# Optimization experiments

Hardware: AMD Instinct MI355X
Metric: run time of the kernel (lower is better)

The kernel has to match this reference:

```python
import jax, jax.numpy as jnp
import numpy as np

B, N, D = 256, 2048, 128
ANCHOR = 0


def setup_inputs() -> dict:
    key = jax.random.key(0)
    k0, k1, k2, k3 = jax.random.split(key, 4)
    return {
        "embs": jax.random.normal(k0, (B * N, D), jnp.float32),
        "W1": jax.random.normal(k1, (D, 2 * D), jnp.float32) / np.sqrt(2 * D),
        "b1": jnp.zeros((D,), jnp.float32),
        "W2": jax.random.normal(k2, (D, D), jnp.float32) / np.sqrt(D),
        "b2": jnp.zeros((D,), jnp.float32),
        "batch_idx": jax.random.randint(k3, (B * N,), 0, B, dtype=jnp.int32),
        "batch_size": B,
        "num_nodes": N,
        "num_anchors": ANCHOR,
    }


def reference(embs, W1, b1, W2, b2, batch_idx, batch_size, num_nodes, num_anchors):
    # static boolean mask over nodes (num_anchors is a Python int)
    non_target = np.arange(num_nodes) != num_anchors
    e = embs.reshape(batch_size, num_nodes, -1)            # (B, N, D)
    non_targets = e[:, non_target]                          # (B, N-1, D)
    target = e[:, ~non_target]                              # (B, 1, D)
    x = jnp.concatenate(
        (jnp.broadcast_to(target, non_targets.shape), non_targets), axis=-1
    )                                                       # (B, N-1, 2D)
    h = jax.nn.relu(jnp.einsum("bnk,dk->bnd", x, W1) + b1)  # (B, N-1, D)
    y = jnp.einsum("bnk,dk->bnd", h, W2) + b2               # (B, N-1, D)
    y = y.reshape(batch_size * (num_nodes - 1), -1)
    bidx = batch_idx.reshape(batch_size, num_nodes)[:, non_target].reshape(-1)
    return jax.ops.segment_sum(y, bidx, num_segments=batch_size)  # (B, D)
```

## Files before the change

kernel.cpp:

```cpp
#include <hip/hip_runtime.h>

#define B_SZ    256
#define N_NODES 2048
#define D_DIM   128
#define NROW_TOT (B_SZ * N_NODES)

typedef __attribute__((ext_vector_type(8))) short short8;
typedef __attribute__((ext_vector_type(4))) float f32x4;

#define WS_W1BF   0
#define WS_COUNT  65536
#define WS_OFF    66560
#define WS_CURSOR 67584
#define WS_ACC    83968
#define WS_P      215040
#define WS_NEEDED (WS_P + NROW_TOT * 4)

__device__ __forceinline__ unsigned pk2(float x, float y) {
    unsigned a = __float_as_uint(x), b = __float_as_uint(y);
    a += 0x7fffu + ((a >> 16) & 1u);
    b += 0x7fffu + ((b >> 16) & 1u);
    return (a >> 16) | (b & 0xffff0000u);
}

__global__ void k_prep_w1(const float* __restrict__ W1, unsigned* __restrict__ w1bf) {
    int i = blockIdx.x * 256 + threadIdx.x;
    float2 f = ((const float2*)W1)[i];
    w1bf[i] = pk2(f.x, f.y);
}

__global__ void k_hist(const int* __restrict__ bidx, int* __restrict__ count) {
    __shared__ int lh[256];
    int t = threadIdx.x;
    lh[t] = 0;
    __syncthreads();
    int base = blockIdx.x * 1024 + t * 4;
    int4 v = ((const int4*)bidx)[blockIdx.x * 256 + t];
    if (((base + 0) & 2047) != 0) atomicAdd(&lh[v.x], 1);
    if (((base + 1) & 2047) != 0) atomicAdd(&lh[v.y], 1);
    if (((base + 2) & 2047) != 0) atomicAdd(&lh[v.z], 1);
    if (((base + 3) & 2047) != 0) atomicAdd(&lh[v.w], 1);
    __syncthreads();
    if (lh[t]) atomicAdd(&count[t], lh[t]);
}

__global__ void k_scan(const int* __restrict__ count, int* __restrict__ off,
                       int* __restrict__ cursor) {
    __shared__ int sv[256];
    int t = threadIdx.x;
    sv[t] = count[t];
    __syncthreads();
    for (int o = 1; o < 256; o <<= 1) {
        int v = (t >= o) ? sv[t - o] : 0;
        __syncthreads();
        sv[t] += v;
        __syncthreads();
    }
    int ex = sv[t] - count[t];
    off[t] = ex;
    cursor[t * 16] = ex;
}

__global__ void k_scatter(const int* __restrict__ bidx, int* __restrict__ cursor,
                          int* __restrict__ P) {
    __shared__ int lh[256];
    __shared__ int sbase[256];
    int t = threadIdx.x;
    lh[t] = 0;
    __syncthreads();
    int base = blockIdx.x * 1024 + t * 4;
    int4 v = ((const int4*)bidx)[blockIdx.x * 256 + t];
    int p0 = -1, p1 = -1, p2 = -1, p3 = -1;
    if (((base + 0) & 2047) != 0) p0 = atomicAdd(&lh[v.x], 1);
    if (((base + 1) & 2047) != 0) p1 = atomicAdd(&lh[v.y], 1);
    if (((base + 2) & 2047) != 0) p2 = atomicAdd(&lh[v.z], 1);
    if (((base + 3) & 2047) != 0) p3 = atomicAdd(&lh[v.w], 1);
    __syncthreads();
    if (lh[t]) sbase[t] = atomicAdd(&cursor[t * 16], lh[t]);
    __syncthreads();
    if (p0 >= 0) P[sbase[v.x] + p0] = base + 0;
    if (p1 >= 0) P[sbase[v.y] + p1] = base + 1;
    if (p2 >= 0) P[sbase[v.z] + p2] = base + 2;
    if (p3 >= 0) P[sbase[v.w] + p3] = base + 3;
}

#define CHUNK   64
#define ESTRIDE 528

__global__ __launch_bounds__(1024) void k_main(
    const float* __restrict__ embs, const float* __restrict__ b1,
    const short* __restrict__ w1bf, const int* __restrict__ P,
    const int* __restrict__ off, const int* __restrict__ count,
    float* __restrict__ ACC)
{
    __shared__ char  estage[CHUNK * ESTRIDE];
    __shared__ float segacc[D_DIM];

    int tid = threadIdx.x;
    int s   = blockIdx.x;
    int cnt = count[s];
    int base = off[s];

    if (tid < D_DIM) segacc[tid] = 0.f;

    int lane = tid & 63;
    int wid  = tid >> 6;
    int rt   = wid & 3;
    int cg   = wid >> 2;
    int q    = lane >> 4;
    int i15  = lane & 15;

    short8 bfrag[8][2];
#pragma unroll
    for (int kt = 0; kt < 8; kt++)
#pragma unroll
        for (int ct = 0; ct < 2; ct++) {
            int n = cg * 32 + ct * 16 + i15;
            bfrag[kt][ct] = *(const short8*)(w1bf + n * 256 + kt * 32 + q * 8);
        }
    float b1c0 = b1[cg * 32 + i15];
    float b1c1 = b1[cg * 32 + 16 + i15];
    float asum0 = 0.f, asum1 = 0.f;

    int srow = tid >> 4;
    int part = tid & 15;
    __syncthreads();

    int nchunk = (cnt + CHUNK - 1) >> 6;
    for (int c = 0; c < nchunk; c++) {
        int rl = c * 64 + srow;
        int gr = base + (rl < cnt ? rl : cnt - 1);
        int ridx = P[gr];
        int b = ridx >> 11;
        const float4* src;
        if (part < 8) src = (const float4*)(embs + (b << 11) * D_DIM) + part * 4;
        else          src = (const float4*)(embs + ridx * D_DIM) + (part - 8) * 4;
        float4 f0 = src[0], f1 = src[1], f2 = src[2], f3 = src[3];
        unsigned u0 = pk2(f0.x, f0.y), u1 = pk2(f0.z, f0.w);
        unsigned u2 = pk2(f1.x, f1.y), u3 = pk2(f1.z, f1.w);
        unsigned u4 = pk2(f2.x, f2.y), u5 = pk2(f2.z, f2.w);
        unsigned u6 = pk2(f3.x, f3.y), u7 = pk2(f3.z, f3.w);
        uint4* dst = (uint4*)(estage + srow * ESTRIDE + part * 32);
        dst[0] = make_uint4(u0, u1, u2, u3);
        dst[1] = make_uint4(u4, u5, u6, u7);
        __syncthreads();

        f32x4 m0 = {0.f, 0.f, 0.f, 0.f}, m1 = {0.f, 0.f, 0.f, 0.f};
        const char* arow = estage + (rt * 16 + i15) * ESTRIDE + q * 16;
#pragma unroll
        for (int kt = 0; kt < 8; kt++) {
            short8 a = *(const short8*)(arow + kt * 64);
            m0 = __builtin_amdgcn_mfma_f32_16x16x32_bf16(a, bfrag[kt][0], m0, 0, 0, 0);
            m1 = __builtin_amdgcn_mfma_f32_16x16x32_bf16(a, bfrag[kt][1], m1, 0, 0, 0);
        }
        int rbase = c * 64 + rt * 16 + q * 4;
#pragma unroll
        for (int j = 0; j < 4; j++) {
            if (rbase + j < cnt) {
                asum0 += fmaxf(m0[j] + b1c0, 0.f);
                asum1 += fmaxf(m1[j] + b1c1, 0.f);
            }
        }
        __syncthreads();
    }

    asum0 += __shfl_xor(asum0, 16, 64);
    asum0 += __shfl_xor(asum0, 32, 64);
    asum1 += __shfl_xor(asum1, 16, 64);
    asum1 += __shfl_xor(asum1, 32, 64);
    if (lane < 16) {
        atomicAdd(&segacc[cg * 32 + lane],      asum0);
        atomicAdd(&segacc[cg * 32 + 16 + lane], asum1);
    }
    __syncthreads();
    if (tid < D_DIM) ACC[s * D_DIM + tid] = segacc[tid];
}

__global__ void k_out(const float* __restrict__ ACC, const float* __restrict__ W2,
                      const float* __restrict__ b2, const int* __restrict__ count,
                      float* __restrict__ out) {
    __shared__ float a[D_DIM];
    int s = blockIdx.x, d = threadIdx.x;
    a[d] = ACC[s * D_DIM + d];
    __syncthreads();
    float sum = (float)count[s] * b2[d];
    const float4* w = (const float4*)(W2 + d * D_DIM);
#pragma unroll
    for (int k = 0; k < 32; k++) {
        float4 wv = w[k];
        sum += a[4 * k + 0] * wv.x + a[4 * k + 1] * wv.y
             + a[4 * k + 2] * wv.z + a[4 * k + 3] * wv.w;
    }
    out[s * D_DIM + d] = sum;
}

extern "C" void kernel_launch(void* const* d_in, const int* in_sizes, int n_in,
                              void* d_out, int out_size, void* d_ws, size_t ws_size,
                              hipStream_t stream) {
    const float* embs = (const float*)d_in[0];
    const float* W1   = (const float*)d_in[1];
    const float* b1   = (const float*)d_in[2];
    const float* W2   = (const float*)d_in[3];
    const float* b2   = (const float*)d_in[4];
    const int*   bidx = (const int*)d_in[5];

    char* ws = (char*)d_ws;
    unsigned* w1bf_u = (unsigned*)(ws + WS_W1BF);
    short*    w1bf   = (short*)(ws + WS_W1BF);
    int*   count  = (int*)(ws + WS_COUNT);
    int*   off    = (int*)(ws + WS_OFF);
    int*   cursor = (int*)(ws + WS_CURSOR);
    float* ACC    = (float*)(ws + WS_ACC);
    int*   P      = (int*)(ws + WS_P);

    hipMemsetAsync(count, 0, 256 * sizeof(int), stream);
    k_prep_w1<<<64, 256, 0, stream>>>(W1, w1bf_u);
    k_hist<<<512, 256, 0, stream>>>(bidx, count);
    k_scan<<<1, 256, 0, stream>>>(count, off, cursor);
    k_scatter<<<512, 256, 0, stream>>>(bidx, cursor, P);
    k_main<<<256, 1024, 0, stream>>>(embs, b1, w1bf, P, off, count, ACC);
    k_out<<<256, 128, 0, stream>>>(ACC, W2, b2, count, (float*)d_out);
}
```

Baseline: 437.3 us.

## Hoist per-batch anchor projection and accumulate segments in shared memory per block

Because the target (anchor) row is shared by every node of a batch, its half of the W1 product is computed once per block and added as a bias, which halves the MFMA K dimension. Each block now streams its own batch's rows contiguously, with no gather. It scatters ReLU outputs into a 256-segment shared-memory accumulator via LDS atomics, which removes the scan/scatter permutation kernels. The anchor row is processed and then subtracted instead of being skipped. Per-block partials (256x256x128 floats) go to scratch and are reduced in k_out. This adds large scratch traffic, LDS atomic contention, and cancellation error from subtracting the anchor contribution.

```diff
diff --git a/kernel.cpp b/kernel.cpp
--- a/kernel.cpp
+++ b/kernel.cpp
@@ -3,24 +3,30 @@
 #define B_SZ    256
 #define N_NODES 2048
 #define D_DIM   128
-#define NROW_TOT (B_SZ * N_NODES)
 
 typedef __attribute__((ext_vector_type(8))) short short8;
 typedef __attribute__((ext_vector_type(4))) float f32x4;
 
-#define WS_W1BF   0
-#define WS_COUNT  65536
-#define WS_OFF    66560
-#define WS_CURSOR 67584
-#define WS_ACC    83968
-#define WS_P      215040
-#define WS_NEEDED (WS_P + NROW_TOT * 4)
+#define WS_W1BF    0
+#define WS_CNT     65536
+#define WS_SCRATCH 66560
 
 __device__ __forceinline__ unsigned pk2(float x, float y) {
     unsigned a = __float_as_uint(x), b = __float_as_uint(y);
     a += 0x7fffu + ((a >> 16) & 1u);
     b += 0x7fffu + ((b >> 16) & 1u);
     return (a >> 16) | (b & 0xffff0000u);
+}
+
+__device__ __forceinline__ short8 pack8(float4 a, float4 b) {
+    union { unsigned u[4]; short8 s; } r;
+    r.u[0] = pk2(a.x, a.y); r.u[1] = pk2(a.z, a.w);
+    r.u[2] = pk2(b.x, b.y); r.u[3] = pk2(b.z, b.w);
+    return r.s;
+}
+
+__device__ __forceinline__ float bf2f(short s) {
+    return __uint_as_float(((unsigned)(unsigned short)s) << 16);
 }
 
 __global__ void k_prep_w1(const float* __restrict__ W1, unsigned* __restrict__ w1bf) {
@@ -44,154 +50,142 @@
     if (lh[t]) atomicAdd(&count[t], lh[t]);
 }
 
-__global__ void k_scan(const int* __restrict__ count, int* __restrict__ off,
-                       int* __restrict__ cursor) {
-    __shared__ int sv[256];
-    int t = threadIdx.x;
-    sv[t] = count[t];
-    __syncthreads();
-    for (int o = 1; o < 256; o <<= 1) {
-        int v = (t >= o) ? sv[t - o] : 0;
-        __syncthreads();
-        sv[t] += v;
-        __syncthreads();
-    }
-    int ex = sv[t] - count[t];
-    off[t] = ex;
-    cursor[t * 16] = ex;
-}
-
-__global__ void k_scatter(const int* __restrict__ bidx, int* __restrict__ cursor,
-                          int* __restrict__ P) {
-    __shared__ int lh[256];
-    __shared__ int sbase[256];
-    int t = threadIdx.x;
-    lh[t] = 0;
-    __syncthreads();
-    int base = blockIdx.x * 1024 + t * 4;
-    int4 v = ((const int4*)bidx)[blockIdx.x * 256 + t];
-    int p0 = -1, p1 = -1, p2 = -1, p3 = -1;
-    if (((base + 0) & 2047) != 0) p0 = atomicAdd(&lh[v.x], 1);
-    if (((base + 1) & 2047) != 0) p1 = atomicAdd(&lh[v.y], 1);
-    if (((base + 2) & 2047) != 0) p2 = atomicAdd(&lh[v.z], 1);
-    if (((base + 3) & 2047) != 0) p3 = atomicAdd(&lh[v.w], 1);
-    __syncthreads();
-    if (lh[t]) sbase[t] = atomicAdd(&cursor[t * 16], lh[t]);
-    __syncthreads();
-    if (p0 >= 0) P[sbase[v.x] + p0] = base + 0;
-    if (p1 >= 0) P[sbase[v.y] + p1] = base + 1;
-    if (p2 >= 0) P[sbase[v.z] + p2] = base + 2;
-    if (p3 >= 0) P[sbase[v.w] + p3] = base + 3;
-}
-
-#define CHUNK   64
-#define ESTRIDE 528
+#define SACC_STRIDE 129
 
 __global__ __launch_bounds__(1024) void k_main(
-    const float* __restrict__ embs, const float* __restrict__ b1,
-    const short* __restrict__ w1bf, const int* __restrict__ P,
-    const int* __restrict__ off, const int* __restrict__ count,
-    float* __restrict__ ACC)
+    const float* __restrict__ embs, const float* __restrict__ W1,
+    const float* __restrict__ b1, const short* __restrict__ w1bf,
+    const int* __restrict__ bidx, float* __restrict__ scratch)
 {
-    __shared__ char  estage[CHUNK * ESTRIDE];
-    __shared__ float segacc[D_DIM];
+    __shared__ float sacc[B_SZ * SACC_STRIDE];
+    __shared__ float tbuf[D_DIM];
+    __shared__ float t2buf[D_DIM];
+    __shared__ float tgtf[D_DIM];
+    __shared__ float tgtb[D_DIM];
 
     int tid = threadIdx.x;
-    int s   = blockIdx.x;
-    int cnt = count[s];
-    int base = off[s];
-
-    if (tid < D_DIM) segacc[tid] = 0.f;
-
-    int lane = tid & 63;
-    int wid  = tid >> 6;
-    int rt   = wid & 3;
-    int cg   = wid >> 2;
-    int q    = lane >> 4;
-    int i15  = lane & 15;
-
-    short8 bfrag[8][2];
-#pragma unroll
-    for (int kt = 0; kt < 8; kt++)
-#pragma unroll
-        for (int ct = 0; ct < 2; ct++) {
-            int n = cg * 32 + ct * 16 + i15;
-            bfrag[kt][ct] = *(const short8*)(w1bf + n * 256 + kt * 32 + q * 8);
+    int b   = blockIdx.x;
+
+    for (int i = tid; i < B_SZ * SACC_STRIDE; i += 1024) sacc[i] = 0.f;
+
+    if (tid < D_DIM) {
+        float v = embs[(b << 11) * D_DIM + tid];
+        tgtf[tid] = v;
+        unsigned ub = __float_as_uint(v);
+        ub += 0x7fffu + ((ub >> 16) & 1u);
+        tgtb[tid] = __uint_as_float(ub & 0xffff0000u);
+    }
+    __syncthreads();
+
+    if (tid < 128) {
+        float s = b1[tid];
+        const float4* w = (const float4*)(W1 + tid * 256);
+#pragma unroll
+        for (int k = 0; k < 32; k++) {
+            float4 wv = w[k];
+            s += tgtf[4 * k + 0] * wv.x + tgtf[4 * k + 1] * wv.y
+               + tgtf[4 * k + 2] * wv.z + tgtf[4 * k + 3] * wv.w;
         }
-    float b1c0 = b1[cg * 32 + i15];
-    float b1c1 = b1[cg * 32 + 16 + i15];
-    float asum0 = 0.f, asum1 = 0.f;
-
-    int srow = tid >> 4;
-    int part = tid & 15;
-    __syncthreads();
-
-    int nchunk = (cnt + CHUNK - 1) >> 6;
-    for (int c = 0; c < nchunk; c++) {
-        int rl = c * 64 + srow;
-        int gr = base + (rl < cnt ? rl : cnt - 1);
-        int ridx = P[gr];
-        int b = ridx >> 11;
-        const float4* src;
-        if (part < 8) src = (const float4*)(embs + (b << 11) * D_DIM) + part * 4;
-        else          src = (const float4*)(embs + ridx * D_DIM) + (part - 8) * 4;
-        float4 f0 = src[0], f1 = src[1], f2 = src[2], f3 = src[3];
-        unsigned u0 = pk2(f0.x, f0.y), u1 = pk2(f0.z, f0.w);
-        unsigned u2 = pk2(f1.x, f1.y), u3 = pk2(f1.z, f1.w);
-        unsigned u4 = pk2(f2.x, f2.y), u5 = pk2(f2.z, f2.w);
-        unsigned u6 = pk2(f3.x, f3.y), u7 = pk2(f3.z, f3.w);
-        uint4* dst = (uint4*)(estage + srow * ESTRIDE + part * 32);
-        dst[0] = make_uint4(u0, u1, u2, u3);
-        dst[1] = make_uint4(u4, u5, u6, u7);
-        __syncthreads();
+        tbuf[tid] = s;
+    } else if (tid < 256) {
+        int d = tid - 128;
+        float s = 0.f;
+        const short8* wr = (const short8*)(w1bf + d * 256 + 128);
+#pragma unroll
+        for (int k8 = 0; k8 < 16; k8++) {
+            short8 v = wr[k8];
+#pragma unroll
+            for (int j = 0; j < 8; j++) s += tgtb[k8 * 8 + j] * bf2f(v[j]);
+        }
+        t2buf[d] = s;
+    }
+    __syncthreads();
+
+    float h_anchor = 0.f;
+    int   seg0 = 0;
+    if (tid < 128) {
+        h_anchor = fmaxf(t2buf[tid] + tbuf[tid], 0.f);
+        seg0 = bidx[b << 11];
+    }
+
+    int lane = tid & 63, wid = tid >> 6;
+    int rt = wid & 3;
+    int cg = wid >> 2;
+    int q = lane >> 4, i15 = lane & 15;
+    int colc = cg * 32 + i15;
+    float tb0 = tbuf[colc], tb1 = tbuf[colc + 16];
+
+    short8 bf[4][2];
+#pragma unroll
+    for (int kt = 0; kt < 4; kt++)
+#pragma unroll
+        for (int ct = 0; ct < 2; ct++)
+            bf[kt][ct] = *(const short8*)(w1bf + (cg * 32 + ct * 16 + i15) * 256
+                                          + 128 + kt * 32 + q * 8);
+
+    const float* abase = embs + ((b << 11) + rt * 16 + i15) * D_DIM + q * 8;
+    int crow = rt * 16 + q * 4;
+    int rbid = (b << 11) + crow;
+
+    for (int it = 0; it < 32; it++) {
+        const float* ap = abase + it * 64 * D_DIM;
+        short8 a0 = pack8(*(const float4*)(ap + 0),  *(const float4*)(ap + 4));
+        short8 a1 = pack8(*(const float4*)(ap + 32), *(const float4*)(ap + 36));
+        short8 a2 = pack8(*(const float4*)(ap + 64), *(const float4*)(ap + 68));
+        short8 a3 = pack8(*(const float4*)(ap + 96), *(const float4*)(ap + 100));
+
+        int r = rbid + it * 64;
+        int s0 = bidx[r], s1 = bidx[r + 1], s2 = bidx[r + 2], s3 = bidx[r + 3];
 
         f32x4 m0 = {0.f, 0.f, 0.f, 0.f}, m1 = {0.f, 0.f, 0.f, 0.f};
-        const char* arow = estage + (rt * 16 + i15) * ESTRIDE + q * 16;
-#pragma unroll
-        for (int kt = 0; kt < 8; kt++) {
-            short8 a = *(const short8*)(arow + kt * 64);
-            m0 = __builtin_amdgcn_mfma_f32_16x16x32_bf16(a, bfrag[kt][0], m0, 0, 0, 0);
-            m1 = __builtin_amdgcn_mfma_f32_16x16x32_bf16(a, bfrag[kt][1], m1, 0, 0, 0);
-        }
-        int rbase = c * 64 + rt * 16 + q * 4;
-#pragma unroll
-        for (int j = 0; j < 4; j++) {
-            if (rbase + j < cnt) {
-                asum0 += fmaxf(m0[j] + b1c0, 0.f);
-                asum1 += fmaxf(m1[j] + b1c1, 0.f);
-            }
-        }
-        __syncthreads();
-    }
-
-    asum0 += __shfl_xor(asum0, 16, 64);
-    asum0 += __shfl_xor(asum0, 32, 64);
-    asum1 += __shfl_xor(asum1, 16, 64);
-    asum1 += __shfl_xor(asum1, 32, 64);
-    if (lane < 16) {
-        atomicAdd(&segacc[cg * 32 + lane],      asum0);
-        atomicAdd(&segacc[cg * 32 + 16 + lane], asum1);
-    }
-    __syncthreads();
-    if (tid < D_DIM) ACC[s * D_DIM + tid] = segacc[tid];
-}
-
-__global__ void k_out(const float* __restrict__ ACC, const float* __restrict__ W2,
+        m0 = __builtin_amdgcn_mfma_f32_16x16x32_bf16(a0, bf[0][0], m0, 0, 0, 0);
+        m1 = __builtin_amdgcn_mfma_f32_16x16x32_bf16(a0, bf[0][1], m1, 0, 0, 0);
+        m0 = __builtin_amdgcn_mfma_f32_16x16x32_bf16(a1, bf[1][0], m0, 0, 0, 0);
+        m1 = __builtin_amdgcn_mfma_f32_16x16x32_bf16(a1, bf[1][1], m1, 0, 0, 0);
+        m0 = __builtin_amdgcn_mfma_f32_16x16x32_bf16(a2, bf[2][0], m0, 0, 0, 0);
+        m1 = __builtin_amdgcn_mfma_f32_16x16x32_bf16(a2, bf[2][1], m1, 0, 0, 0);
+        m0 = __builtin_amdgcn_mfma_f32_16x16x32_bf16(a3, bf[3][0], m0, 0, 0, 0);
+        m1 = __builtin_amdgcn_mfma_f32_16x16x32_bf16(a3, bf[3][1], m1, 0, 0, 0);
+
+        atomicAdd(&sacc[s0 * SACC_STRIDE + colc],      fmaxf(m0[0] + tb0, 0.f));
+        atomicAdd(&sacc[s0 * SACC_STRIDE + colc + 16], fmaxf(m1[0] + tb1, 0.f));
+        atomicAdd(&sacc[s1 * SACC_STRIDE + colc],      fmaxf(m0[1] + tb0, 0.f));
+        atomicAdd(&sacc[s1 * SACC_STRIDE + colc + 16], fmaxf(m1[1] + tb1, 0.f));
+        atomicAdd(&sacc[s2 * SACC_STRIDE + colc],      fmaxf(m0[2] + tb0, 0.f));
+        atomicAdd(&sacc[s2 * SACC_STRIDE + colc + 16], fmaxf(m1[2] + tb1, 0.f));
+        atomicAdd(&sacc[s3 * SACC_STRIDE + colc],      fmaxf(m0[3] + tb0, 0.f));
+        atomicAdd(&sacc[s3 * SACC_STRIDE + colc + 16], fmaxf(m1[3] + tb1, 0.f));
+    }
+    __syncthreads();
+
+    if (tid < 128) atomicAdd(&sacc[seg0 * SACC_STRIDE + tid], -h_anchor);
+    __syncthreads();
+
+    float* dst = scratch + b * (B_SZ * D_DIM);
+    for (int i = tid; i < B_SZ * D_DIM; i += 1024)
+        dst[i] = sacc[(i >> 7) * SACC_STRIDE + (i & 127)];
+}
+
+__global__ void k_out(const float* __restrict__ scratch, const float* __restrict__ W2,
                       const float* __restrict__ b2, const int* __restrict__ count,
                       float* __restrict__ out) {
     __shared__ float a[D_DIM];
     int s = blockIdx.x, d = threadIdx.x;
-    a[d] = ACC[s * D_DIM + d];
-    __syncthreads();
-    float sum = (float)count[s] * b2[d];
+    float sum = 0.f;
+    const float* p = scratch + s * D_DIM + d;
+#pragma unroll 4
+    for (int blk = 0; blk < 256; blk++) sum += p[blk * (B_SZ * D_DIM)];
+    a[d] = sum;
+    __syncthreads();
+    float o = (float)count[s] * b2[d];
     const float4* w = (const float4*)(W2 + d * D_DIM);
 #pragma unroll
     for (int k = 0; k < 32; k++) {
         float4 wv = w[k];
-        sum += a[4 * k + 0] * wv.x + a[4 * k + 1] * wv.y
-             + a[4 * k + 2] * wv.z + a[4 * k + 3] * wv.w;
-    }
-    out[s * D_DIM + d] = sum;
+        o += a[4 * k + 0] * wv.x + a[4 * k + 1] * wv.y
+           + a[4 * k + 2] * wv.z + a[4 * k + 3] * wv.w;
+    }
+    out[s * D_DIM + d] = o;
 }
 
 extern "C" void kernel_launch(void* const* d_in, const int* in_sizes, int n_in,
@@ -205,19 +199,14 @@
     const int*   bidx = (const int*)d_in[5];
 
     char* ws = (char*)d_ws;
-    unsigned* w1bf_u = (unsigned*)(ws + WS_W1BF);
-    short*    w1bf   = (short*)(ws + WS_W1BF);
-    int*   count  = (int*)(ws + WS_COUNT);
-    int*   off    = (int*)(ws + WS_OFF);
-    int*   cursor = (int*)(ws + WS_CURSOR);
-    float* ACC    = (float*)(ws + WS_ACC);
-    int*   P      = (int*)(ws + WS_P);
+    unsigned* w1bf_u  = (unsigned*)(ws + WS_W1BF);
+    short*    w1bf    = (short*)(ws + WS_W1BF);
+    int*      count   = (int*)(ws + WS_CNT);
+    float*    scratch = (float*)(ws + WS_SCRATCH);
 
     hipMemsetAsync(count, 0, 256 * sizeof(int), stream);
     k_prep_w1<<<64, 256, 0, stream>>>(W1, w1bf_u);
     k_hist<<<512, 256, 0, stream>>>(bidx, count);
-    k_scan<<<1, 256, 0, stream>>>(count, off, cursor);
-    k_scatter<<<512, 256, 0, stream>>>(bidx, cursor, P);
-    k_main<<<256, 1024, 0, stream>>>(embs, b1, w1bf, P, off, count, ACC);
-    k_out<<<256, 128, 0, stream>>>(ACC, W2, b2, count, (float*)d_out);
-}
+    k_main<<<256, 1024, 0, stream>>>(embs, W1, b1, w1bf, bidx, scratch);
+    k_out<<<256, 128, 0, stream>>>(scratch, W2, b2, count, (float*)d_out);
+}
```

After: 659.6 us. +50.8%, slower.
